# Kernel tuning notes

Measured on AMD Instinct MI355X. Metric: run time of the kernel, lower is better.

The kernel has to match this reference:

```python
import jax, jax.numpy as jnp
import numpy as np

D_MODEL = 2048
N_HEADS = 16
N_KV = 4
D_HEAD = D_MODEL // N_HEADS
N_GROUPS = N_HEADS // N_KV
THETA = 10000.0


def bitlinear(x, W):
    """BitNet b1.58 BitLinear: ternary weights (absmean scale) + 8-bit absmax activations (STE)."""
    sw = jnp.mean(jnp.abs(W)) + 1e-5
    Wq = jnp.clip(jnp.round(W / sw), -1.0, 1.0) * sw
    sx = 127.0 / jnp.clip(jnp.max(jnp.abs(x), axis=-1, keepdims=True), 1e-5, None)
    xq = jnp.clip(jnp.round(x * sx), -128.0, 127.0) / sx
    return jnp.einsum('bsd,od->bso', xq, Wq)


def rope_tables(seq, d_head, dtype=jnp.float32):
    freqs = 1.0 / (THETA ** (jnp.arange(0, d_head, 2, dtype=dtype) / d_head))
    t = jnp.arange(seq, dtype=dtype)
    ang = jnp.outer(t, freqs)  # [seq, d_head//2]
    return jnp.cos(ang), jnp.sin(ang)


def apply_rope(x, cos, sin):
    # x: [b, h, s, d]; cos/sin: [s, d//2] -> broadcast [1,1,s,d//2]
    c = cos[None, None]
    s = sin[None, None]
    x1, x2 = jnp.split(x, 2, axis=-1)
    return jnp.concatenate([x1 * c - x2 * s, x2 * c + x1 * s], axis=-1)


def setup_inputs() -> dict:
    key = jax.random.key(0)
    ks = jax.random.split(key, 5)
    return {
        'x': jax.random.normal(ks[0], (2, 2048, D_MODEL), jnp.float32),
        'Wq': jax.random.normal(ks[1], (D_MODEL, D_MODEL), jnp.float32) * 0.02,
        'Wk': jax.random.normal(ks[2], (N_KV * D_HEAD, D_MODEL), jnp.float32) * 0.02,
        'Wv': jax.random.normal(ks[3], (N_KV * D_HEAD, D_MODEL), jnp.float32) * 0.02,
        'Wo': jax.random.normal(ks[4], (D_MODEL, D_MODEL), jnp.float32) * 0.02,
    }


def reference(x, Wq, Wk, Wv, Wo):
    b, s, _ = x.shape
    q = bitlinear(x, Wq).reshape(b, s, N_HEADS, D_HEAD).transpose(0, 2, 1, 3)
    k = bitlinear(x, Wk).reshape(b, s, N_KV, D_HEAD).transpose(0, 2, 1, 3)
    v = bitlinear(x, Wv).reshape(b, s, N_KV, D_HEAD).transpose(0, 2, 1, 3)
    cos, sin = rope_tables(s, D_HEAD)
    q = apply_rope(q, cos, sin)
    k = apply_rope(k, cos, sin)
    # GQA without materializing expanded K/V: group query heads per kv head
    qg = q.reshape(b, N_KV, N_GROUPS, s, D_HEAD)
    scale = 1.0 / jnp.sqrt(jnp.asarray(D_HEAD, x.dtype))
    scores = jnp.einsum('bkgsd,bktd->bkgst', qg, k) * scale  # [b,kv,g,s,s]
    causal = jnp.triu(jnp.ones((s, s), dtype=bool), k=1)
    scores = jnp.where(causal[None, None, None], jnp.asarray(-jnp.inf, scores.dtype), scores)
    p = jax.nn.softmax(scores, axis=-1)
    out = jnp.einsum('bkgst,bktd->bkgsd', p, v)  # [b,kv,g,s,d]
    out = out.reshape(b, N_HEADS, s, D_HEAD).transpose(0, 2, 1, 3).reshape(b, s, D_MODEL)
    return bitlinear(out, Wo)
```

## Files before the change

kernel.cpp:

```cpp
#include <hip/hip_runtime.h>
#include <hip/hip_bf16.h>
#include <stdint.h>

typedef __bf16 bf16x8 __attribute__((ext_vector_type(8)));
typedef float f32x4 __attribute__((ext_vector_type(4)));
typedef unsigned short u16x8 __attribute__((ext_vector_type(8)));
typedef unsigned short u16x4 __attribute__((ext_vector_type(4)));

__device__ __forceinline__ unsigned short f2bf(float f) {
  union { float f; unsigned int u; } v; v.f = f;
  unsigned int r = v.u + 0x7fffu + ((v.u >> 16) & 1u);
  return (unsigned short)(r >> 16);
}

__device__ __forceinline__ f32x4 mfma16(bf16x8 a, bf16x8 b, f32x4 c) {
  return __builtin_amdgcn_mfma_f32_16x16x32_bf16(a, b, c, 0, 0, 0);
}

__device__ __forceinline__ void gload_lds16(const void* g, void* l) {
  __builtin_amdgcn_global_load_lds(
      (const __attribute__((address_space(1))) void*)g,
      (__attribute__((address_space(3))) void*)l, 16, 0, 0);
}

__global__ void absum_k(const float* __restrict__ w, long n4, float* __restrict__ out) {
  long i = (long)blockIdx.x * blockDim.x + threadIdx.x;
  long stride = (long)gridDim.x * blockDim.x;
  const float4* w4 = (const float4*)w;
  float s = 0.f;
  for (; i < n4; i += stride) {
    float4 v = w4[i];
    s += fabsf(v.x) + fabsf(v.y) + fabsf(v.z) + fabsf(v.w);
  }
  #pragma unroll
  for (int o = 32; o; o >>= 1) s += __shfl_down(s, o);
  __shared__ float sm[4];
  int lane = threadIdx.x & 63, wv = threadIdx.x >> 6;
  if (lane == 0) sm[wv] = s;
  __syncthreads();
  if (threadIdx.x == 0) atomicAdd(out, sm[0] + sm[1] + sm[2] + sm[3]);
}

__global__ void finalize_k(const float* __restrict__ sums, float* __restrict__ sw) {
  int i = threadIdx.x;
  if (i < 4) {
    const float inv[4] = {1.f/(2048.f*2048.f), 1.f/(512.f*2048.f),
                          1.f/(512.f*2048.f), 1.f/(2048.f*2048.f)};
    sw[i] = sums[i] * inv[i] + 1e-5f;
  }
}

__global__ void quantw_k(const float* __restrict__ w, unsigned short* __restrict__ o,
                         long n4, const float* __restrict__ swp) {
  float sw = *swp;
  long i = (long)blockIdx.x * blockDim.x + threadIdx.x;
  long stride = (long)gridDim.x * blockDim.x;
  const float4* w4 = (const float4*)w;
  u16x4* o4 = (u16x4*)o;
  for (; i < n4; i += stride) {
    float4 v = w4[i];
    u16x4 t;
    t[0] = f2bf(fminf(fmaxf(rintf(v.x / sw), -1.f), 1.f));
    t[1] = f2bf(fminf(fmaxf(rintf(v.y / sw), -1.f), 1.f));
    t[2] = f2bf(fminf(fmaxf(rintf(v.z / sw), -1.f), 1.f));
    t[3] = f2bf(fminf(fmaxf(rintf(v.w / sw), -1.f), 1.f));
    o4[i] = t;
  }
}

__global__ void ropetab_k(float* __restrict__ cosT, float* __restrict__ sinT) {
  int idx = blockIdx.x * 256 + threadIdx.x;
  int s = idx >> 6, d = idx & 63;
  float freq = expf(-(float)d * (9.210340371976184f / 64.0f));
  float ang = (float)s * freq;
  cosT[idx] = cosf(ang);
  sinT[idx] = sinf(ang);
}

__global__ __launch_bounds__(256) void quanta_k(const float* __restrict__ x,
                                                unsigned short* __restrict__ xq,
                                                float* __restrict__ rs) {
  int row = blockIdx.x;
  const float* xr = x + (size_t)row * 2048;
  int tid = threadIdx.x;
  float4 v0 = ((const float4*)xr)[tid * 2];
  float4 v1 = ((const float4*)xr)[tid * 2 + 1];
  float m = fmaxf(fmaxf(fmaxf(fabsf(v0.x), fabsf(v0.y)), fmaxf(fabsf(v0.z), fabsf(v0.w))),
                  fmaxf(fmaxf(fabsf(v1.x), fabsf(v1.y)), fmaxf(fabsf(v1.z), fabsf(v1.w))));
  #pragma unroll
  for (int o = 32; o; o >>= 1) m = fmaxf(m, __shfl_xor(m, o));
  __shared__ float sm[4];
  if ((tid & 63) == 0) sm[tid >> 6] = m;
  __syncthreads();
  m = fmaxf(fmaxf(sm[0], sm[1]), fmaxf(sm[2], sm[3]));
  float rm = fmaxf(m, 1e-5f);
  float sx = 127.0f / rm;
  float vv[8] = {v0.x, v0.y, v0.z, v0.w, v1.x, v1.y, v1.z, v1.w};
  u16x8 o8;
  #pragma unroll
  for (int j = 0; j < 8; j++) {
    float r = rintf(vv[j] * sx);
    r = fminf(fmaxf(r, -128.f), 127.f);
    o8[j] = f2bf(r);
  }
  ((u16x8*)(xq + (size_t)row * 2048))[tid] = o8;
  if (tid == 0) rs[row] = rm * (1.0f / 127.0f);
}

__global__ __launch_bounds__(256) void gemm_k(const unsigned short* __restrict__ A,
                                              const unsigned short* __restrict__ Bt,
                                              float* __restrict__ C,
                                              int M, int N, int K,
                                              const float* __restrict__ rowscale,
                                              const float* __restrict__ sw, int mode) {
  __shared__ unsigned short As[128 * 32];
  __shared__ unsigned short Bs[128 * 32];
  int tid = threadIdx.x;
  int lane = tid & 63, wv = tid >> 6;
  int g = lane >> 4, li = lane & 15;
  int wm = wv >> 1, wn = wv & 1;
  int m0 = blockIdx.y * 128, n0 = blockIdx.x * 128;
  int sr = lane >> 2;
  int sc = lane & 3;
  int gc = (sc ^ ((sr >> 1) & 3)) * 8;
  int swz = (g ^ ((li >> 1) & 3)) * 8;
  f32x4 acc[4][4] = {};

  for (int k0 = 0; k0 < K; k0 += 32) {
    __syncthreads();
    #pragma unroll
    for (int j = 0; j < 2; j++) {
      int row = (wv * 2 + j) * 16 + sr;
      gload_lds16(&A[(size_t)(m0 + row) * K + k0 + gc], &As[(wv * 2 + j) * 512]);
      gload_lds16(&Bt[(size_t)(n0 + row) * K + k0 + gc], &Bs[(wv * 2 + j) * 512]);
    }
    __syncthreads();
    bf16x8 af[4], bfr[4];
    #pragma unroll
    for (int i = 0; i < 4; i++)
      af[i] = *(const bf16x8*)&As[(wm * 64 + i * 16 + li) * 32 + swz];
    #pragma unroll
    for (int j = 0; j < 4; j++)
      bfr[j] = *(const bf16x8*)&Bs[(wn * 64 + j * 16 + li) * 32 + swz];
    #pragma unroll
    for (int i = 0; i < 4; i++)
      #pragma unroll
      for (int j = 0; j < 4; j++)
        acc[i][j] = mfma16(af[i], bfr[j], acc[i][j]);
  }

  #pragma unroll
  for (int i = 0; i < 4; i++) {
    int row = m0 + wm * 64 + i * 16 + g * 4;
    #pragma unroll
    for (int j = 0; j < 4; j++) {
      int col = n0 + wn * 64 + j * 16 + li;
      float s = (mode == 0) ? ((col < 2048) ? sw[0] : (col < 2560 ? sw[1] : sw[2]))
                            : sw[3];
      #pragma unroll
      for (int r = 0; r < 4; r++)
        C[(size_t)(row + r) * N + col] = acc[i][j][r] * (rowscale[row + r] * s);
    }
  }
}

__global__ __launch_bounds__(256) void ropeapply_k(const float* __restrict__ raw,
                                                   const float* __restrict__ cosT,
                                                   const float* __restrict__ sinT,
                                                   unsigned short* __restrict__ qb,
                                                   unsigned short* __restrict__ kb,
                                                   unsigned short* __restrict__ vtb) {
  int r = blockIdx.x;
  int b = r >> 11, s = r & 2047;
  const float* row = raw + (size_t)r * 3072;
  int tid = threadIdx.x;
  for (int idx = tid; idx < 1024; idx += 256) {
    int h = idx >> 6, d = idx & 63;
    float x1 = row[h * 128 + d], x2 = row[h * 128 + d + 64];
    float c = cosT[s * 64 + d], sn = sinT[s * 64 + d];
    size_t base = ((size_t)(b * 16 + h) * 2048 + s) * 128;
    qb[base + d]      = f2bf(x1 * c - x2 * sn);
    qb[base + d + 64] = f2bf(x2 * c + x1 * sn);
  }
  {
    int h = tid >> 6, d = tid & 63;
    float x1 = row[2048 + h * 128 + d], x2 = row[2048 + h * 128 + d + 64];
    float c = cosT[s * 64 + d], sn = sinT[s * 64 + d];
    size_t base = ((size_t)(b * 4 + h) * 2048 + s) * 128;
    kb[base + d]      = f2bf(x1 * c - x2 * sn);
    kb[base + d + 64] = f2bf(x2 * c + x1 * sn);
  }
  for (int idx = tid; idx < 512; idx += 256) {
    int h = idx >> 7, d = idx & 127;
    vtb[((size_t)(b * 4 + h) * 128 + d) * 2048 + s] = f2bf(row[2560 + idx]);
  }
}

__global__ __launch_bounds__(256) void attn_k(const unsigned short* __restrict__ qb,
                                              const unsigned short* __restrict__ kb,
                                              const unsigned short* __restrict__ vtb,
                                              float* __restrict__ out) {
  int h = blockIdx.y, b = blockIdx.z;
  int wv = threadIdx.x >> 6, lane = threadIdx.x & 63;
  int g = lane >> 4, li = lane & 15;
  int kh = h >> 2;
  const unsigned short* qp = qb + ((size_t)(b * 16 + h) * 2048) * 128;
  const unsigned short* kp = kb + ((size_t)(b * 4 + kh) * 2048) * 128;
  const unsigned short* vp = vtb + ((size_t)(b * 4 + kh) * 128) * 2048;

  __shared__ unsigned short Ks[64 * 128];
  __shared__ unsigned short Vs[128 * 64];
  __shared__ unsigned short Pl[4][16][72];

  const float cs = 0.1275356234f;

  #pragma unroll 1
  for (int part = 0; part < 2; ++part) {
    int tq = part ? (31 - blockIdx.x) : blockIdx.x;
    int qw = tq * 64 + wv * 16;
    bf16x8 qf[4];
    #pragma unroll
    for (int kk = 0; kk < 4; kk++)
      qf[kk] = *(const bf16x8*)&qp[(size_t)(qw + li) * 128 + kk * 32 + g * 8];
    f32x4 oacc[8] = {};
    float mrun = -INFINITY, lrun = 0.f;
    int nt = tq + 1;
    for (int t = 0; t < nt; ++t) {
      int kv0 = t * 64;
      __syncthreads();
      #pragma unroll
      for (int i = 0; i < 4; i++) {
        int r = wv * 16 + i * 4 + g;
        gload_lds16(kp + (size_t)(kv0 + r) * 128 + ((li ^ (r & 7)) * 8),
                    &Ks[(wv * 16 + i * 4) * 128]);
      }
      #pragma unroll
      for (int i = 0; i < 4; i++) {
        int d = wv * 32 + i * 8 + (lane >> 3);
        int c = lane & 7;
        gload_lds16(vp + (size_t)d * 2048 + kv0 + ((c ^ (d & 7)) * 8),
                    &Vs[(wv * 32 + i * 8) * 64]);
      }
      __syncthreads();
      f32x4 st[4] = {};
      #pragma unroll
      for (int kk = 0; kk < 4; kk++) {
        #pragma unroll
        for (int n = 0; n < 4; n++) {
          bf16x8 kf = *(const bf16x8*)&Ks[(n * 16 + li) * 128 +
                                          (((kk * 4 + g) ^ (li & 7)) * 8)];
          st[n] = mfma16(kf, qf[kk], st[n]);
        }
      }
      int qrel = (t == nt - 1) ? (qw + li - kv0) : (1 << 30);
      float mx = -INFINITY;
      #pragma unroll
      for (int n = 0; n < 4; n++)
        #pragma unroll
        for (int r = 0; r < 4; r++) {
          float v = st[n][r] * cs;
          v = ((n * 16 + g * 4 + r) > qrel) ? -INFINITY : v;
          st[n][r] = v;
          mx = fmaxf(mx, v);
        }
      mx = fmaxf(mx, __shfl_xor(mx, 16));
      mx = fmaxf(mx, __shfl_xor(mx, 32));
      float mnew = fmaxf(mrun, mx);
      float alpha = exp2f(mrun - mnew);
      float lsum = 0.f;
      #pragma unroll
      for (int n = 0; n < 4; n++) {
        u16x4 pw;
        #pragma unroll
        for (int r = 0; r < 4; r++) {
          float p = exp2f(st[n][r] - mnew);
          lsum += p;
          pw[r] = f2bf(p);
        }
        *(u16x4*)&Pl[wv][li][n * 16 + g * 4] = pw;
      }
      lsum += __shfl_xor(lsum, 16);
      lsum += __shfl_xor(lsum, 32);
      lrun = lrun * alpha + lsum;
      mrun = mnew;
      if (__any(alpha != 1.0f)) {
        float ar[4];
        #pragma unroll
        for (int r = 0; r < 4; r++) ar[r] = __shfl(alpha, g * 4 + r, 64);
        #pragma unroll
        for (int dn = 0; dn < 8; dn++)
          #pragma unroll
          for (int r = 0; r < 4; r++) oacc[dn][r] *= ar[r];
      }
      __builtin_amdgcn_wave_barrier();
      bf16x8 pa0 = *(const bf16x8*)&Pl[wv][li][g * 8];
      bf16x8 pa1 = *(const bf16x8*)&Pl[wv][li][32 + g * 8];
      #pragma unroll
      for (int dn = 0; dn < 8; dn++) {
        int d = dn * 16 + li;
        bf16x8 vf0 = *(const bf16x8*)&Vs[d * 64 + ((g ^ (li & 7)) * 8)];
        bf16x8 vf1 = *(const bf16x8*)&Vs[d * 64 + (((4 + g) ^ (li & 7)) * 8)];
        oacc[dn] = mfma16(pa0, vf0, oacc[dn]);
        oacc[dn] = mfma16(pa1, vf1, oacc[dn]);
      }
      __builtin_amdgcn_wave_barrier();
    }
    float linv = 1.0f / lrun;
    float lr_[4];
    #pragma unroll
    for (int r = 0; r < 4; r++) lr_[r] = __shfl(linv, g * 4 + r, 64);
    size_t obase = ((size_t)(b * 2048 + qw + g * 4)) * 2048 + h * 128;
    #pragma unroll
    for (int dn = 0; dn < 8; dn++)
      #pragma unroll
      for (int r = 0; r < 4; r++)
        out[obase + (size_t)r * 2048 + dn * 16 + li] = oacc[dn][r] * lr_[r];
  }
}

extern "C" void kernel_launch(void* const* d_in, const int* in_sizes, int n_in,
                              void* d_out, int out_size, void* d_ws, size_t ws_size,
                              hipStream_t stream) {
  const float* x  = (const float*)d_in[0];
  const float* Wq = (const float*)d_in[1];
  const float* Wk = (const float*)d_in[2];
  const float* Wv = (const float*)d_in[3];
  const float* Wo = (const float*)d_in[4];
  float* out = (float*)d_out;

  char* ws = (char*)d_ws;
  size_t off = 0;
  auto alloc = [&](size_t bytes) -> void* {
    void* p = ws + off;
    off = (off + bytes + 255) & ~(size_t)255;
    return p;
  };
  float* sums = (float*)alloc(16);
  float* sw   = (float*)alloc(16);
  float* rs   = (float*)alloc(4096 * 4);
  float* rs2  = (float*)alloc(4096 * 4);
  float* cosT = (float*)alloc((size_t)131072 * 4);
  float* sinT = (float*)alloc((size_t)131072 * 4);
  unsigned short* Wcat = (unsigned short*)alloc((size_t)3072 * 2048 * 2);
  unsigned short* Wot  = (unsigned short*)alloc((size_t)2048 * 2048 * 2);
  unsigned short* qb   = (unsigned short*)alloc((size_t)2 * 16 * 2048 * 128 * 2);
  unsigned short* kb   = (unsigned short*)alloc((size_t)2 * 4 * 2048 * 128 * 2);
  unsigned short* vtb  = (unsigned short*)alloc((size_t)2 * 4 * 128 * 2048 * 2);
  unsigned short* xq   = (unsigned short*)alloc((size_t)4096 * 2048 * 2);
  float* raw  = (float*)alloc((size_t)4096 * 3072 * 4);
  float* attn = raw;

  hipMemsetAsync(sums, 0, 16, stream);
  absum_k<<<256, 256, 0, stream>>>(Wq, (long)2048 * 2048 / 4, sums + 0);
  absum_k<<<128, 256, 0, stream>>>(Wk, (long)512 * 2048 / 4, sums + 1);
  absum_k<<<128, 256, 0, stream>>>(Wv, (long)512 * 2048 / 4, sums + 2);
  absum_k<<<256, 256, 0, stream>>>(Wo, (long)2048 * 2048 / 4, sums + 3);
  finalize_k<<<1, 4, 0, stream>>>(sums, sw);
  quantw_k<<<512, 256, 0, stream>>>(Wq, Wcat, (long)2048 * 2048 / 4, sw + 0);
  quantw_k<<<128, 256, 0, stream>>>(Wk, Wcat + (size_t)2048 * 2048, (long)512 * 2048 / 4, sw + 1);
  quantw_k<<<128, 256, 0, stream>>>(Wv, Wcat + (size_t)2560 * 2048, (long)512 * 2048 / 4, sw + 2);
  quantw_k<<<512, 256, 0, stream>>>(Wo, Wot, (long)2048 * 2048 / 4, sw + 3);
  ropetab_k<<<512, 256, 0, stream>>>(cosT, sinT);
  quanta_k<<<4096, 256, 0, stream>>>(x, xq, rs);
  dim3 g1(3072 / 128, 4096 / 128);
  gemm_k<<<g1, 256, 0, stream>>>(xq, Wcat, raw, 4096, 3072, 2048, rs, sw, 0);
  ropeapply_k<<<4096, 256, 0, stream>>>(raw, cosT, sinT, qb, kb, vtb);
  attn_k<<<dim3(16, 16, 2), 256, 0, stream>>>(qb, kb, vtb, attn);
  quanta_k<<<4096, 256, 0, stream>>>(attn, xq, rs2);
  dim3 g2(2048 / 128, 4096 / 128);
  gemm_k<<<g2, 256, 0, stream>>>(xq, Wot, out, 4096, 2048, 2048, rs2, sw, 1);
}
```

Before: 404.3 us.

## Double-buffer attention K/V loads, LDS-transpose V, swizzle GEMM blocks

Result: faster. 386.6 us (-4.4%).

```diff
diff --git a/kernel.cpp b/kernel.cpp
--- a/kernel.cpp
+++ b/kernel.cpp
@@ -3,6 +3,7 @@
 #include <stdint.h>
 
 typedef __bf16 bf16x8 __attribute__((ext_vector_type(8)));
+typedef __bf16 bf16x4v __attribute__((ext_vector_type(4)));
 typedef float f32x4 __attribute__((ext_vector_type(4)));
 typedef unsigned short u16x8 __attribute__((ext_vector_type(8)));
 typedef unsigned short u16x4 __attribute__((ext_vector_type(4)));
@@ -119,7 +120,10 @@
   int lane = tid & 63, wv = tid >> 6;
   int g = lane >> 4, li = lane & 15;
   int wm = wv >> 1, wn = wv & 1;
-  int m0 = blockIdx.y * 128, n0 = blockIdx.x * 128;
+  int L = blockIdx.x + gridDim.x * blockIdx.y;
+  int nwg = gridDim.x * gridDim.y;
+  int swz_id = (L & 7) * (nwg >> 3) + (L >> 3);
+  int m0 = (swz_id / gridDim.x) * 128, n0 = (swz_id % gridDim.x) * 128;
   int sr = lane >> 2;
   int sc = lane & 3;
   int gc = (sc ^ ((sr >> 1) & 3)) * 8;
@@ -168,8 +172,8 @@
                                                    const float* __restrict__ cosT,
                                                    const float* __restrict__ sinT,
                                                    unsigned short* __restrict__ qb,
-                                                   unsigned short* __restrict__ kb,
-                                                   unsigned short* __restrict__ vtb) {
+                                                   unsigned short* __restrict__ kb) {
+  const float CS = 0.1275356234f;
   int r = blockIdx.x;
   int b = r >> 11, s = r & 2047;
   const float* row = raw + (size_t)r * 3072;
@@ -179,8 +183,8 @@
     float x1 = row[h * 128 + d], x2 = row[h * 128 + d + 64];
     float c = cosT[s * 64 + d], sn = sinT[s * 64 + d];
     size_t base = ((size_t)(b * 16 + h) * 2048 + s) * 128;
-    qb[base + d]      = f2bf(x1 * c - x2 * sn);
-    qb[base + d + 64] = f2bf(x2 * c + x1 * sn);
+    qb[base + d]      = f2bf((x1 * c - x2 * sn) * CS);
+    qb[base + d + 64] = f2bf((x2 * c + x1 * sn) * CS);
   }
   {
     int h = tid >> 6, d = tid & 63;
@@ -190,9 +194,32 @@
     kb[base + d]      = f2bf(x1 * c - x2 * sn);
     kb[base + d + 64] = f2bf(x2 * c + x1 * sn);
   }
-  for (int idx = tid; idx < 512; idx += 256) {
-    int h = idx >> 7, d = idx & 127;
-    vtb[((size_t)(b * 4 + h) * 128 + d) * 2048 + s] = f2bf(row[2560 + idx]);
+}
+
+__global__ __launch_bounds__(256) void transv_k(const float* __restrict__ raw,
+                                                unsigned short* __restrict__ vtb) {
+  __shared__ unsigned short T[128][136];
+  int sc = blockIdx.x, hk = blockIdx.y, b = blockIdx.z;
+  int tid = threadIdx.x;
+  #pragma unroll
+  for (int i = 0; i < 16; i++) {
+    int idx4 = i * 256 + tid;
+    int s = idx4 >> 5, d4 = idx4 & 31;
+    float4 v = *(const float4*)&raw[((size_t)(b * 2048 + sc * 128 + s)) * 3072 +
+                                    2560 + hk * 128 + d4 * 4];
+    u16x4 t4;
+    t4[0] = f2bf(v.x); t4[1] = f2bf(v.y); t4[2] = f2bf(v.z); t4[3] = f2bf(v.w);
+    *(u16x4*)&T[s][d4 * 4] = t4;
+  }
+  __syncthreads();
+  int d = tid >> 1, s0 = (tid & 1) * 64;
+  size_t obase = ((size_t)(b * 4 + hk) * 128 + d) * 2048 + sc * 128 + s0;
+  #pragma unroll
+  for (int j = 0; j < 8; j++) {
+    u16x8 o8;
+    #pragma unroll
+    for (int e = 0; e < 8; e++) o8[e] = T[s0 + j * 8 + e][d];
+    *(u16x8*)&vtb[obase + j * 8] = o8;
   }
 }
 
@@ -208,15 +235,13 @@
   const unsigned short* kp = kb + ((size_t)(b * 4 + kh) * 2048) * 128;
   const unsigned short* vp = vtb + ((size_t)(b * 4 + kh) * 128) * 2048;
 
-  __shared__ unsigned short Ks[64 * 128];
-  __shared__ unsigned short Vs[128 * 64];
+  __shared__ unsigned short Ks[2][64 * 128];
+  __shared__ unsigned short Vs[2][128 * 64];
   __shared__ unsigned short Pl[4][16][72];
-
-  const float cs = 0.1275356234f;
 
   #pragma unroll 1
   for (int part = 0; part < 2; ++part) {
-    int tq = part ? (31 - blockIdx.x) : blockIdx.x;
+    int tq = part ? (31 - (int)blockIdx.x) : (int)blockIdx.x;
     int qw = tq * 64 + wv * 16;
     bf16x8 qf[4];
     #pragma unroll
@@ -225,44 +250,69 @@
     f32x4 oacc[8] = {};
     float mrun = -INFINITY, lrun = 0.f;
     int nt = tq + 1;
-    for (int t = 0; t < nt; ++t) {
-      int kv0 = t * 64;
-      __syncthreads();
+
+    {
       #pragma unroll
       for (int i = 0; i < 4; i++) {
         int r = wv * 16 + i * 4 + g;
-        gload_lds16(kp + (size_t)(kv0 + r) * 128 + ((li ^ (r & 7)) * 8),
-                    &Ks[(wv * 16 + i * 4) * 128]);
+        gload_lds16(kp + (size_t)r * 128 + ((li ^ (r & 7)) * 8),
+                    &Ks[0][(wv * 16 + i * 4) * 128]);
       }
       #pragma unroll
       for (int i = 0; i < 4; i++) {
         int d = wv * 32 + i * 8 + (lane >> 3);
-        int c = lane & 7;
-        gload_lds16(vp + (size_t)d * 2048 + kv0 + ((c ^ (d & 7)) * 8),
-                    &Vs[(wv * 32 + i * 8) * 64]);
-      }
-      __syncthreads();
+        gload_lds16(vp + (size_t)d * 2048 + (((lane & 7) ^ (d & 7)) * 8),
+                    &Vs[0][(wv * 32 + i * 8) * 64]);
+      }
+    }
+
+    #pragma unroll 1
+    for (int t = 0; t < nt; ++t) {
+      int cur = t & 1;
+      if (t + 1 < nt) {
+        int kv1 = (t + 1) * 64;
+        #pragma unroll
+        for (int i = 0; i < 4; i++) {
+          int r = wv * 16 + i * 4 + g;
+          gload_lds16(kp + (size_t)(kv1 + r) * 128 + ((li ^ (r & 7)) * 8),
+                      &Ks[cur ^ 1][(wv * 16 + i * 4) * 128]);
+        }
+        #pragma unroll
+        for (int i = 0; i < 4; i++) {
+          int d = wv * 32 + i * 8 + (lane >> 3);
+          gload_lds16(vp + (size_t)d * 2048 + kv1 + (((lane & 7) ^ (d & 7)) * 8),
+                      &Vs[cur ^ 1][(wv * 32 + i * 8) * 64]);
+        }
+        asm volatile("s_waitcnt vmcnt(8)" ::: "memory");
+      } else {
+        asm volatile("s_waitcnt vmcnt(0)" ::: "memory");
+      }
+      __builtin_amdgcn_s_barrier();
+      asm volatile("" ::: "memory");
+
       f32x4 st[4] = {};
       #pragma unroll
       for (int kk = 0; kk < 4; kk++) {
         #pragma unroll
         for (int n = 0; n < 4; n++) {
-          bf16x8 kf = *(const bf16x8*)&Ks[(n * 16 + li) * 128 +
-                                          (((kk * 4 + g) ^ (li & 7)) * 8)];
+          bf16x8 kf = *(const bf16x8*)&Ks[cur][(n * 16 + li) * 128 +
+                                              (((kk * 4 + g) ^ (li & 7)) * 8)];
           st[n] = mfma16(kf, qf[kk], st[n]);
         }
       }
-      int qrel = (t == nt - 1) ? (qw + li - kv0) : (1 << 30);
-      float mx = -INFINITY;
+      if (t == nt - 1) {
+        int qrel = qw + li - t * 64;
+        #pragma unroll
+        for (int n = 0; n < 4; n++)
+          #pragma unroll
+          for (int r = 0; r < 4; r++)
+            if ((n * 16 + g * 4 + r) > qrel) st[n][r] = -INFINITY;
+      }
+      float mx = st[0][0];
       #pragma unroll
       for (int n = 0; n < 4; n++)
         #pragma unroll
-        for (int r = 0; r < 4; r++) {
-          float v = st[n][r] * cs;
-          v = ((n * 16 + g * 4 + r) > qrel) ? -INFINITY : v;
-          st[n][r] = v;
-          mx = fmaxf(mx, v);
-        }
+        for (int r = 0; r < 4; r++) mx = fmaxf(mx, st[n][r]);
       mx = fmaxf(mx, __shfl_xor(mx, 16));
       mx = fmaxf(mx, __shfl_xor(mx, 32));
       float mnew = fmaxf(mrun, mx);
@@ -270,14 +320,14 @@
       float lsum = 0.f;
       #pragma unroll
       for (int n = 0; n < 4; n++) {
-        u16x4 pw;
+        bf16x4v pw;
         #pragma unroll
         for (int r = 0; r < 4; r++) {
           float p = exp2f(st[n][r] - mnew);
           lsum += p;
-          pw[r] = f2bf(p);
+          pw[r] = (__bf16)p;
         }
-        *(u16x4*)&Pl[wv][li][n * 16 + g * 4] = pw;
+        *(bf16x4v*)&Pl[wv][li][n * 16 + g * 4] = pw;
       }
       lsum += __shfl_xor(lsum, 16);
       lsum += __shfl_xor(lsum, 32);
@@ -298,12 +348,15 @@
       #pragma unroll
       for (int dn = 0; dn < 8; dn++) {
         int d = dn * 16 + li;
-        bf16x8 vf0 = *(const bf16x8*)&Vs[d * 64 + ((g ^ (li & 7)) * 8)];
-        bf16x8 vf1 = *(const bf16x8*)&Vs[d * 64 + (((4 + g) ^ (li & 7)) * 8)];
+        bf16x8 vf0 = *(const bf16x8*)&Vs[cur][d * 64 + ((g ^ (li & 7)) * 8)];
+        bf16x8 vf1 = *(const bf16x8*)&Vs[cur][d * 64 + (((4 + g) ^ (li & 7)) * 8)];
         oacc[dn] = mfma16(pa0, vf0, oacc[dn]);
         oacc[dn] = mfma16(pa1, vf1, oacc[dn]);
       }
       __builtin_amdgcn_wave_barrier();
+      asm volatile("" ::: "memory");
+      __builtin_amdgcn_s_barrier();
+      asm volatile("" ::: "memory");
     }
     float linv = 1.0f / lrun;
     float lr_[4];
@@ -364,7 +417,8 @@
   quanta_k<<<4096, 256, 0, stream>>>(x, xq, rs);
   dim3 g1(3072 / 128, 4096 / 128);
   gemm_k<<<g1, 256, 0, stream>>>(xq, Wcat, raw, 4096, 3072, 2048, rs, sw, 0);
-  ropeapply_k<<<4096, 256, 0, stream>>>(raw, cosT, sinT, qb, kb, vtb);
+  ropeapply_k<<<4096, 256, 0, stream>>>(raw, cosT, sinT, qb, kb);
+  transv_k<<<dim3(16, 4, 2), 256, 0, stream>>>(raw, vtb);
   attn_k<<<dim3(16, 16, 2), 256, 0, stream>>>(qb, kb, vtb, attn);
   quanta_k<<<4096, 256, 0, stream>>>(attn, xq, rs2);
   dim3 g2(2048 / 128, 4096 / 128);
```
